# Performance work log

Hardware: AMD Instinct MI355X
Metric: run time of the kernel (lower is better)

The kernel has to match this reference:

```python
import jax, jax.numpy as jnp
import numpy as np

B, D_MODEL, N, H = 4, 256, 2048, 4
DIM = D_MODEL // H  # 64


def setup_inputs() -> dict:
    k = jax.random.key(0)
    ks = jax.random.split(k, 11)
    mk = lambda kk, shape, s=1.0: jax.random.normal(kk, shape, dtype=jnp.float32) * s
    return {
        'query': mk(ks[0], (B, D_MODEL, N)),
        'key': mk(ks[1], (B, D_MODEL, N)),
        'value': mk(ks[2], (B, D_MODEL, N)),
        # 1x1 Conv1d == per-position linear: weight [out, in], bias [out]
        'wq': mk(ks[3], (D_MODEL, D_MODEL), 0.05), 'bq': mk(ks[4], (D_MODEL,), 0.05),
        'wk': mk(ks[5], (D_MODEL, D_MODEL), 0.05), 'bk': mk(ks[6], (D_MODEL,), 0.05),
        'wv': mk(ks[7], (D_MODEL, D_MODEL), 0.05), 'bv': mk(ks[8], (D_MODEL,), 0.05),
        'wm': mk(ks[9], (D_MODEL, D_MODEL), 0.05), 'bm': mk(ks[10], (D_MODEL,), 0.05),
    }


def _proj(x, w, b):
    # Conv1d(kernel_size=1): [b, c_in, n] -> [b, c_out, n]
    return jnp.einsum('oc,bcn->bon', w, x) + b[None, :, None]


def reference(query, key, value, wq, bq, wk, bk, wv, bv, wm, bm):
    b = query.shape[0]
    # project and split channels d_model -> (dim, h); matches torch .view(b, dim, h, -1)
    q = _proj(query, wq, bq).reshape(b, DIM, H, -1)
    kk = _proj(key, wk, bk).reshape(b, DIM, H, -1)
    v = _proj(value, wv, bv).reshape(b, DIM, H, -1)
    scores = jnp.einsum('bdhn,bdhm->bhnm', q, kk) / jnp.sqrt(jnp.float32(DIM))
    prob = jax.nn.softmax(scores, axis=-1)  # [b, h, n, m]
    x = jnp.einsum('bhnm,bdhm->bdhn', prob, v)
    return _proj(x.reshape(b, DIM * H, -1), wm, bm)
```

## Files before the change

kernel.cpp:

```cpp
#include <hip/hip_runtime.h>
#include <hip/hip_bf16.h>

#define DMODEL 256
#define NSEQ   2048
#define NB     4
#define NH     4
#define DHEAD  64

typedef __attribute__((ext_vector_type(8))) short short8;
typedef __attribute__((ext_vector_type(4))) float float4v;
typedef __attribute__((ext_vector_type(2))) float float2v;
typedef __attribute__((ext_vector_type(2))) unsigned int uint2v;
typedef unsigned short u16;

#define AS1 __attribute__((address_space(1)))
#define AS3 __attribute__((address_space(3)))

static __device__ inline u16 f2bf(float f) {
    unsigned u = __builtin_bit_cast(unsigned, f);
    u += 0x7fffu + ((u >> 16) & 1u);
    return (u16)(u >> 16);
}
static __device__ inline unsigned pack2bf(float a, float b) {
    return (unsigned)f2bf(a) | ((unsigned)f2bf(b) << 16);
}
static __device__ inline float max3f(float a, float b, float c) {
    return fmaxf(fmaxf(a, b), c);
}
static __device__ inline float tmax16(const float4v* s) {
    float a = max3f(s[0][0], s[0][1], s[0][2]);
    float b = max3f(s[0][3], s[1][0], s[1][1]);
    float c = max3f(s[1][2], s[1][3], s[2][0]);
    float d = max3f(s[2][1], s[2][2], s[2][3]);
    float e = max3f(s[3][0], s[3][1], s[3][2]);
    float f = max3f(a, b, c);
    float g = max3f(d, e, s[3][3]);
    return fmaxf(f, g);
}

__global__ __launch_bounds__(256) void prep_kernel(
    const float* __restrict__ xq, const float* __restrict__ xk,
    const float* __restrict__ xv,
    const float* __restrict__ wq, const float* __restrict__ wk,
    const float* __restrict__ wv, const float* __restrict__ wm,
    u16* __restrict__ xt_ws, u16* __restrict__ wbf)
{
    const int bid = blockIdx.x;
    const int tid = threadIdx.x;

    if (bid >= 1536) {
        const int id = bid - 1536;
        const int sr = id & 255, m = id >> 8;
        const float* W = (m == 0) ? wq : (m == 1) ? wk : (m == 2) ? wv : wm;
        float v;
        if (m < 3) {
            int og = (sr & ~15) | ((sr & 3) << 2) | ((sr >> 2) & 3);
            v = W[(size_t)og * DMODEL + tid];
        } else {
            int c = ((tid & 63) << 2) | (tid >> 6);
            v = W[(size_t)sr * DMODEL + c];
        }
        wbf[(size_t)m * 65536 + (size_t)sr * DMODEL + tid] = f2bf(v);
        return;
    }

    const int nt = bid & 31;
    const int ct = (bid >> 5) & 3;
    const int z  = bid >> 7;
    const int b = z / 3, mode = z % 3;
    const float* X = ((mode == 0) ? xq : (mode == 1) ? xk : xv) + (size_t)b * DMODEL * NSEQ;
    u16* dst = xt_ws + (size_t)z * NSEQ * DMODEL;

    __shared__ u16 t[64][72];

    #pragma unroll
    for (int i = 0; i < 4; i++) {
        int e = tid + i * 256;
        int c = e >> 4;
        int n4 = (e & 15) * 4;
        float4v v = *(const float4v*)&X[(size_t)(ct * 64 + c) * NSEQ + nt * 64 + n4];
        #pragma unroll
        for (int j = 0; j < 4; j++) {
            int row = n4 + j;
            int fr = (row & 7) ^ ((row >> 3) & 7);
            t[row][(((c >> 3) ^ fr) << 3) + (c & 7)] = f2bf(v[j]);
        }
    }
    __syncthreads();
    #pragma unroll
    for (int i = 0; i < 4; i++) {
        int e = tid + i * 256;
        int n = e >> 4;
        int cb = (e & 15) * 4;
        int fr = (n & 7) ^ ((n >> 3) & 7);
        uint2v val = *(const uint2v*)&t[n][(((cb >> 3) ^ fr) << 3) + (cb & 7)];
        *(uint2v*)&dst[(size_t)(nt * 64 + n) * DMODEL + ct * 64 + cb] = val;
    }
}

__global__ __launch_bounds__(256) void proj_qkv_kernel(
    const u16* __restrict__ xt_ws, const u16* __restrict__ wbf,
    const float* __restrict__ bqp, const float* __restrict__ bkp, const float* __restrict__ bvp,
    u16* __restrict__ q_ws, u16* __restrict__ k_ws, u16* __restrict__ vt_ws)
{
    const int nt0 = blockIdx.x, ot = blockIdx.y, bz = blockIdx.z;
    const int b = bz / 3, mode = bz % 3;
    const float* BI = (mode == 0) ? bqp : (mode == 1) ? bkp : bvp;

    const int tid = threadIdx.x;
    const int wave = tid >> 6, lane = tid & 63;
    const int g = lane >> 4, ql = lane & 15;
    const int srow8 = lane >> 3, su = lane & 7;
    const int u_l = su ^ srow8;
    const int obase = ot * 64, nbase = nt0 * 64;

    const u16* Asrc = wbf + (size_t)mode * 65536;
    const u16* Bsrc = xt_ws + (size_t)bz * (NSEQ * DMODEL);

    __shared__ u16 at[2][64][64];
    __shared__ u16 bt[2][64][64];

    float4v acc[4];
    #pragma unroll
    for (int i = 0; i < 4; i++) acc[i] = (float4v){0.f, 0.f, 0.f, 0.f};

    #define PSTAGE(bufi_, c0_)                                                         \
        { _Pragma("unroll")                                                            \
          for (int p_ = 0; p_ < 2; p_++) {                                             \
            int rb_ = wave * 8 + p_ * 32;                                              \
            int row_ = rb_ + srow8;                                                    \
            __builtin_amdgcn_global_load_lds(                                          \
                (const AS1 unsigned int*)(Asrc + (size_t)(obase + row_) * DMODEL + (c0_) + u_l * 8), \
                (AS3 unsigned int*)&at[bufi_][rb_][0], 16, 0, 0);                      \
            __builtin_amdgcn_global_load_lds(                                          \
                (const AS1 unsigned int*)(Bsrc + (size_t)(nbase + row_) * DMODEL + (c0_) + u_l * 8), \
                (AS3 unsigned int*)&bt[bufi_][rb_][0], 16, 0, 0);                      \
          } }

    PSTAGE(0, 0)
    __syncthreads();
    int buf = 0;
    const int sw = ql & 7;
    #pragma unroll
    for (int t = 0; t < 4; t++) {
        if (t < 3) PSTAGE(buf ^ 1, (t + 1) * 64)
        #pragma unroll
        for (int kc = 0; kc < 2; kc++) {
            short8 afrag = *(const short8*)&at[buf][wave * 16 + ql][(((kc * 4 + g) ^ sw)) * 8];
            #pragma unroll
            for (int nt = 0; nt < 4; nt++) {
                short8 bfrag = *(const short8*)&bt[buf][nt * 16 + ql][(((kc * 4 + g) ^ sw)) * 8];
                acc[nt] = __builtin_amdgcn_mfma_f32_16x16x32_bf16(afrag, bfrag, acc[nt], 0, 0, 0);
            }
        }
        __syncthreads();
        buf ^= 1;
    }
    #undef PSTAGE

    const int h = g;
    const int d0 = (obase + wave * 16) >> 2;
    float bias[4];
    #pragma unroll
    for (int r = 0; r < 4; r++) bias[r] = BI[obase + wave * 16 + 4 * r + g];

    #pragma unroll
    for (int nt = 0; nt < 4; nt++) {
        int n = nbase + nt * 16 + ql;
        float v[4];
        #pragma unroll
        for (int r = 0; r < 4; r++) v[r] = acc[nt][r] + bias[r];
        if (mode == 0) {
            #pragma unroll
            for (int r = 0; r < 4; r++) v[r] *= 0.18033688011112042f;
            uint2v pk = {pack2bf(v[0], v[1]), pack2bf(v[2], v[3])};
            *(uint2v*)&q_ws[((size_t)(b * NH + h) * NSEQ + n) * DHEAD + d0] = pk;
        } else if (mode == 1) {
            uint2v pk = {pack2bf(v[0], v[1]), pack2bf(v[2], v[3])};
            *(uint2v*)&k_ws[((size_t)(b * NH + h) * NSEQ + n) * DHEAD + d0] = pk;
        } else {
            #pragma unroll
            for (int r = 0; r < 4; r++)
                vt_ws[((size_t)(b * NH + h) * DHEAD + d0 + r) * NSEQ + n] = f2bf(v[r]);
        }
    }
}

__global__ __launch_bounds__(512) void attn_kernel(
    const u16* __restrict__ q_ws, const u16* __restrict__ k_ws,
    const u16* __restrict__ vt_ws, float* __restrict__ part_ws,
    float* __restrict__ ml_ws)
{
    const int bid = blockIdx.x;
    const int orig = (bid & 7) * 64 + (bid >> 3);
    const int bh = orig >> 5;
    const int qt128 = (orig >> 1) & 15;
    const int half = orig & 1;
    const int tid = threadIdx.x;
    const int wave = tid >> 6, lane = tid & 63;
    const int g = lane >> 4, ql = lane & 15;
    const int qbase = qt128 * 128 + wave * 16;

    const u16* qp = q_ws + ((size_t)bh * NSEQ + qbase) * DHEAD;
    const u16* kp = k_ws + (size_t)bh * NSEQ * DHEAD + (size_t)half * 1024 * DHEAD;
    const u16* vp = vt_ws + (size_t)bh * DHEAD * NSEQ;
    const int voff = half * 1024;

    __shared__ u16 kt[2][64][64];
    __shared__ u16 vt[2][64][64];
    __shared__ u16 p_lds[8][16][72];

    const int srow = lane >> 3;
    const int su_l = lane & 7;
    const int u_l  = su_l ^ srow;
    const int swz  = ql & 7;

    short8 qf[2];
    #pragma unroll
    for (int kc = 0; kc < 2; kc++)
        qf[kc] = *(const short8*)(qp + (size_t)ql * DHEAD + kc * 32 + g * 8);

    float4v acc[4];
    #pragma unroll
    for (int t = 0; t < 4; t++) acc[t] = (float4v){0.f, 0.f, 0.f, 0.f};
    float mrun = -INFINITY, lrun = 0.f;

    #define STAGE(mb_, bufi_)                                                          \
        {                                                                              \
            int row_ = wave * 8 + srow;                                                \
            __builtin_amdgcn_global_load_lds(                                          \
                (const AS1 unsigned int*)(kp + (size_t)((mb_) + row_) * DHEAD + u_l * 8), \
                (AS3 unsigned int*)&kt[bufi_][wave * 8][0], 16, 0, 0);                 \
            __builtin_amdgcn_global_load_lds(                                          \
                (const AS1 unsigned int*)(vp + (size_t)row_ * NSEQ + voff + (mb_) + u_l * 8), \
                (AS3 unsigned int*)&vt[bufi_][wave * 8][0], 16, 0, 0);                 \
        }

    STAGE(0, 0);
    __syncthreads();

    int buf = 0;
    for (int t = 0; t < 16; t++) {
        const int mb = t * 64;
        if (t < 15) STAGE(mb + 64, buf ^ 1);

        float4v st[4];
        #pragma unroll
        for (int mt = 0; mt < 4; mt++) st[mt] = (float4v){0.f, 0.f, 0.f, 0.f};
        #pragma unroll
        for (int mt = 0; mt < 4; mt++) {
            #pragma unroll
            for (int kc = 0; kc < 2; kc++) {
                short8 kf = *(const short8*)&kt[buf][mt * 16 + ql][((kc * 4 + g) ^ swz) * 8];
                st[mt] = __builtin_amdgcn_mfma_f32_16x16x32_bf16(kf, qf[kc], st[mt], 0, 0, 0);
            }
        }

        float tmax = tmax16(&st[0]);
        tmax = fmaxf(tmax, __shfl_xor(tmax, 16, 64));
        tmax = fmaxf(tmax, __shfl_xor(tmax, 32, 64));

        if (__any(tmax > mrun + 8.f)) {
            float mnew = fmaxf(mrun, tmax);
            float a = __builtin_amdgcn_exp2f(mrun - mnew);
            #pragma unroll
            for (int tt = 0; tt < 4; tt++)
                #pragma unroll
                for (int r = 0; r < 4; r++) acc[tt][r] *= a;
            lrun *= a;
            mrun = mnew;
        }

        float psum = 0.f;
        #pragma unroll
        for (int mt = 0; mt < 4; mt++) {
            float p0 = __builtin_amdgcn_exp2f(st[mt][0] - mrun);
            float p1 = __builtin_amdgcn_exp2f(st[mt][1] - mrun);
            float p2 = __builtin_amdgcn_exp2f(st[mt][2] - mrun);
            float p3 = __builtin_amdgcn_exp2f(st[mt][3] - mrun);
            psum += (p0 + p1) + (p2 + p3);
            *(uint2v*)&p_lds[wave][ql][mt * 16 + g * 4] = (uint2v){pack2bf(p0, p1), pack2bf(p2, p3)};
        }
        psum += __shfl_xor(psum, 16, 64);
        psum += __shfl_xor(psum, 32, 64);
        lrun += psum;

        #pragma unroll
        for (int kc = 0; kc < 2; kc++) {
            short8 pf = *(const short8*)&p_lds[wave][ql][kc * 32 + g * 8];
            #pragma unroll
            for (int tt = 0; tt < 4; tt++) {
                short8 vf = *(const short8*)&vt[buf][tt * 16 + ql][((kc * 4 + g) ^ swz) * 8];
                acc[tt] = __builtin_amdgcn_mfma_f32_16x16x32_bf16(vf, pf, acc[tt], 0, 0, 0);
            }
        }
        __syncthreads();
        buf ^= 1;
    }
    #undef STAGE

    float* prow = part_ws + ((size_t)(half * 16 + bh) * NSEQ + qbase + ql) * 64;
    #pragma unroll
    for (int t = 0; t < 4; t++)
        *(float4v*)&prow[t * 16 + g * 4] = acc[t];
    if (g == 0) {
        *(float2v*)&ml_ws[((size_t)(half * 16 + bh) * NSEQ + qbase + ql) * 2] =
            (float2v){mrun, lrun};
    }
}

__global__ __launch_bounds__(256) void proj_out_kernel(
    const float* __restrict__ part_ws, const float* __restrict__ ml_ws,
    const u16* __restrict__ wbf, const float* __restrict__ bm,
    float* __restrict__ out)
{
    const int nt0 = blockIdx.x, ot = blockIdx.y, b = blockIdx.z;

    const int tid = threadIdx.x;
    const int wave = tid >> 6, lane = tid & 63;
    const int g = lane >> 4, ql = lane & 15;
    const int srow8 = lane >> 3, su = lane & 7;
    const int u_l = su ^ srow8;
    const int obase = ot * 64, nbase = nt0 * 64;

    const u16* Asrc = wbf + (size_t)3 * 65536;

    __shared__ u16 at[64][64];
    __shared__ u16 bt[64][64];

    float4v acc[4];
    #pragma unroll
    for (int i = 0; i < 4; i++) acc[i] = (float4v){0.f, 0.f, 0.f, 0.f};

    const int rrow = tid >> 2;
    const int qcol = tid & 3;
    const int sw = ql & 7;

    #pragma unroll
    for (int t = 0; t < 4; t++) {
        const int c0 = t * 64;
        __syncthreads();
        #pragma unroll
        for (int p_ = 0; p_ < 2; p_++) {
            int rb_ = wave * 8 + p_ * 32;
            int row_ = rb_ + srow8;
            __builtin_amdgcn_global_load_lds(
                (const AS1 unsigned int*)(Asrc + (size_t)(obase + row_) * DMODEL + c0 + u_l * 8),
                (AS3 unsigned int*)&at[rb_][0], 16, 0, 0);
        }
        {
            const int bh = b * NH + t;
            const int n = nbase + rrow;
            const float* p0 = part_ws + ((size_t)bh * NSEQ + n) * 64;
            const float* p1 = part_ws + ((size_t)(16 + bh) * NSEQ + n) * 64;
            float2v ml0 = *(const float2v*)&ml_ws[((size_t)bh * NSEQ + n) * 2];
            float2v ml1 = *(const float2v*)&ml_ws[((size_t)(16 + bh) * NSEQ + n) * 2];
            float mM = fmaxf(ml0[0], ml1[0]);
            float e0 = __builtin_amdgcn_exp2f(ml0[0] - mM);
            float e1 = __builtin_amdgcn_exp2f(ml1[0] - mM);
            float inv = 1.f / (ml0[1] * e0 + ml1[1] * e1);
            float s0 = e0 * inv, s1 = e1 * inv;
            #pragma unroll
            for (int j = 0; j < 4; j++) {
                int cb = qcol * 16 + j * 4;
                float4v f0 = *(const float4v*)&p0[cb];
                float4v f1 = *(const float4v*)&p1[cb];
                float x0 = f0[0] * s0 + f1[0] * s1;
                float x1 = f0[1] * s0 + f1[1] * s1;
                float x2 = f0[2] * s0 + f1[2] * s1;
                float x3 = f0[3] * s0 + f1[3] * s1;
                *(uint2v*)&bt[rrow][(((cb >> 3) ^ (rrow & 7)) << 3) + (cb & 7)] =
                    (uint2v){pack2bf(x0, x1), pack2bf(x2, x3)};
            }
        }
        __syncthreads();
        #pragma unroll
        for (int kc = 0; kc < 2; kc++) {
            short8 afrag = *(const short8*)&at[wave * 16 + ql][(((kc * 4 + g) ^ sw)) * 8];
            #pragma unroll
            for (int nt = 0; nt < 4; nt++) {
                short8 bfrag = *(const short8*)&bt[nt * 16 + ql][(((kc * 4 + g) ^ sw)) * 8];
                acc[nt] = __builtin_amdgcn_mfma_f32_16x16x32_bf16(afrag, bfrag, acc[nt], 0, 0, 0);
            }
        }
    }

    const int o0 = obase + wave * 16 + g * 4;
    #pragma unroll
    for (int nt = 0; nt < 4; nt++) {
        int n = nbase + nt * 16 + ql;
        #pragma unroll
        for (int r = 0; r < 4; r++) {
            int o = o0 + r;
            out[((size_t)b * DMODEL + o) * NSEQ + n] = acc[nt][r] + bm[o];
        }
    }
}

extern "C" void kernel_launch(void* const* d_in, const int* in_sizes, int n_in,
                              void* d_out, int out_size, void* d_ws, size_t ws_size,
                              hipStream_t stream)
{
    const float* query = (const float*)d_in[0];
    const float* key   = (const float*)d_in[1];
    const float* value = (const float*)d_in[2];
    const float* wq = (const float*)d_in[3];
    const float* bq = (const float*)d_in[4];
    const float* wk = (const float*)d_in[5];
    const float* bk = (const float*)d_in[6];
    const float* wv = (const float*)d_in[7];
    const float* bv = (const float*)d_in[8];
    const float* wm = (const float*)d_in[9];
    const float* bm = (const float*)d_in[10];
    float* out = (float*)d_out;

    char* ws = (char*)d_ws;
    const size_t SEG = (size_t)NB * NH * NSEQ * DHEAD * sizeof(u16);
    u16*   q_ws    = (u16*)(ws);
    u16*   k_ws    = (u16*)(ws + SEG);
    u16*   vt_ws   = (u16*)(ws + 2 * SEG);
    float* part_ws = (float*)(ws + 3 * SEG);
    float* ml_ws   = (float*)(ws + 3 * SEG + (size_t)2 * 16 * NSEQ * 64 * sizeof(float));
    char*  after_ml = ws + 3 * SEG + (size_t)2 * 16 * NSEQ * 64 * sizeof(float)
                         + (size_t)2 * 16 * NSEQ * 2 * sizeof(float);
    u16*   xt_ws   = (u16*)(after_ml);
    u16*   wbf     = (u16*)(after_ml + (size_t)12 * NSEQ * DMODEL * sizeof(u16));

    prep_kernel<<<dim3(2560), 256, 0, stream>>>(
        query, key, value, wq, wk, wv, wm, xt_ws, wbf);
    proj_qkv_kernel<<<dim3(32, 4, 12), 256, 0, stream>>>(
        xt_ws, wbf, bq, bk, bv, q_ws, k_ws, vt_ws);
    attn_kernel<<<dim3(512), 512, 0, stream>>>(q_ws, k_ws, vt_ws, part_ws, ml_ws);
    proj_out_kernel<<<dim3(32, 4, NB), 256, 0, stream>>>(part_ws, ml_ws, wbf, bm, out);
}
```

Before: 146.4 us.

## Split KV into quarters and give each wave two query tiles

The attention kernel now splits the key sequence four ways instead of two and launches 1024 blocks of 4 waves instead of 512 blocks of 8 waves. Each wave handles 32 query rows as two 16-row tiles, so every K/V fragment read from LDS feeds two MFMAs. The output projection merges four partial softmax results instead of two. The aim is better LDS reuse and more parallelism, at the cost of twice the partial-result traffic, a larger workspace and more registers per wave.

Measured after the change: 160.4 us. 9.5% more time.

```diff
diff --git a/kernel.cpp b/kernel.cpp
--- a/kernel.cpp
+++ b/kernel.cpp
@@ -186,112 +186,140 @@
     }
 }
 
-__global__ __launch_bounds__(512) void attn_kernel(
+__global__ __launch_bounds__(256) void attn_kernel(
     const u16* __restrict__ q_ws, const u16* __restrict__ k_ws,
     const u16* __restrict__ vt_ws, float* __restrict__ part_ws,
     float* __restrict__ ml_ws)
 {
     const int bid = blockIdx.x;
-    const int orig = (bid & 7) * 64 + (bid >> 3);
-    const int bh = orig >> 5;
-    const int qt128 = (orig >> 1) & 15;
-    const int half = orig & 1;
+    const int orig = (bid & 7) * 128 + (bid >> 3);
+    const int bh = orig >> 6;
+    const int qt128 = (orig >> 2) & 15;
+    const int quarter = orig & 3;
     const int tid = threadIdx.x;
     const int wave = tid >> 6, lane = tid & 63;
     const int g = lane >> 4, ql = lane & 15;
-    const int qbase = qt128 * 128 + wave * 16;
+    const int qbase = qt128 * 128 + wave * 32;
 
     const u16* qp = q_ws + ((size_t)bh * NSEQ + qbase) * DHEAD;
-    const u16* kp = k_ws + (size_t)bh * NSEQ * DHEAD + (size_t)half * 1024 * DHEAD;
+    const u16* kp = k_ws + (size_t)bh * NSEQ * DHEAD + (size_t)quarter * 512 * DHEAD;
     const u16* vp = vt_ws + (size_t)bh * DHEAD * NSEQ;
-    const int voff = half * 1024;
+    const int voff = quarter * 512;
 
     __shared__ u16 kt[2][64][64];
     __shared__ u16 vt[2][64][64];
-    __shared__ u16 p_lds[8][16][72];
+    __shared__ u16 p_lds[4][2][16][72];
 
     const int srow = lane >> 3;
     const int su_l = lane & 7;
     const int u_l  = su_l ^ srow;
     const int swz  = ql & 7;
 
-    short8 qf[2];
-    #pragma unroll
-    for (int kc = 0; kc < 2; kc++)
-        qf[kc] = *(const short8*)(qp + (size_t)ql * DHEAD + kc * 32 + g * 8);
-
-    float4v acc[4];
-    #pragma unroll
-    for (int t = 0; t < 4; t++) acc[t] = (float4v){0.f, 0.f, 0.f, 0.f};
-    float mrun = -INFINITY, lrun = 0.f;
+    short8 qf[2][2];
+    #pragma unroll
+    for (int qt = 0; qt < 2; qt++)
+        #pragma unroll
+        for (int kc = 0; kc < 2; kc++)
+            qf[qt][kc] = *(const short8*)(qp + (size_t)(qt * 16 + ql) * DHEAD + kc * 32 + g * 8);
+
+    float4v acc[2][4];
+    #pragma unroll
+    for (int qt = 0; qt < 2; qt++)
+        #pragma unroll
+        for (int t = 0; t < 4; t++) acc[qt][t] = (float4v){0.f, 0.f, 0.f, 0.f};
+    float m0 = -INFINITY, m1 = -INFINITY, l0 = 0.f, l1 = 0.f;
 
     #define STAGE(mb_, bufi_)                                                          \
         {                                                                              \
-            int row_ = wave * 8 + srow;                                                \
-            __builtin_amdgcn_global_load_lds(                                          \
-                (const AS1 unsigned int*)(kp + (size_t)((mb_) + row_) * DHEAD + u_l * 8), \
-                (AS3 unsigned int*)&kt[bufi_][wave * 8][0], 16, 0, 0);                 \
-            __builtin_amdgcn_global_load_lds(                                          \
-                (const AS1 unsigned int*)(vp + (size_t)row_ * NSEQ + voff + (mb_) + u_l * 8), \
-                (AS3 unsigned int*)&vt[bufi_][wave * 8][0], 16, 0, 0);                 \
+            _Pragma("unroll")                                                          \
+            for (int i_ = 0; i_ < 2; i_++) {                                           \
+                int row_ = wave * 16 + i_ * 8 + srow;                                  \
+                __builtin_amdgcn_global_load_lds(                                      \
+                    (const AS1 unsigned int*)(kp + (size_t)((mb_) + row_) * DHEAD + u_l * 8), \
+                    (AS3 unsigned int*)&kt[bufi_][wave * 16 + i_ * 8][0], 16, 0, 0);   \
+                __builtin_amdgcn_global_load_lds(                                      \
+                    (const AS1 unsigned int*)(vp + (size_t)row_ * NSEQ + voff + (mb_) + u_l * 8), \
+                    (AS3 unsigned int*)&vt[bufi_][wave * 16 + i_ * 8][0], 16, 0, 0);   \
+            }                                                                          \
         }
 
     STAGE(0, 0);
     __syncthreads();
 
     int buf = 0;
-    for (int t = 0; t < 16; t++) {
+    for (int t = 0; t < 8; t++) {
         const int mb = t * 64;
-        if (t < 15) STAGE(mb + 64, buf ^ 1);
-
-        float4v st[4];
-        #pragma unroll
-        for (int mt = 0; mt < 4; mt++) st[mt] = (float4v){0.f, 0.f, 0.f, 0.f};
+        if (t < 7) STAGE(mb + 64, buf ^ 1);
+
+        float4v st[2][4];
+        #pragma unroll
+        for (int qt = 0; qt < 2; qt++)
+            #pragma unroll
+            for (int mt = 0; mt < 4; mt++) st[qt][mt] = (float4v){0.f, 0.f, 0.f, 0.f};
         #pragma unroll
         for (int mt = 0; mt < 4; mt++) {
             #pragma unroll
             for (int kc = 0; kc < 2; kc++) {
                 short8 kf = *(const short8*)&kt[buf][mt * 16 + ql][((kc * 4 + g) ^ swz) * 8];
-                st[mt] = __builtin_amdgcn_mfma_f32_16x16x32_bf16(kf, qf[kc], st[mt], 0, 0, 0);
-            }
-        }
-
-        float tmax = tmax16(&st[0]);
-        tmax = fmaxf(tmax, __shfl_xor(tmax, 16, 64));
-        tmax = fmaxf(tmax, __shfl_xor(tmax, 32, 64));
-
-        if (__any(tmax > mrun + 8.f)) {
-            float mnew = fmaxf(mrun, tmax);
-            float a = __builtin_amdgcn_exp2f(mrun - mnew);
+                st[0][mt] = __builtin_amdgcn_mfma_f32_16x16x32_bf16(kf, qf[0][kc], st[0][mt], 0, 0, 0);
+                st[1][mt] = __builtin_amdgcn_mfma_f32_16x16x32_bf16(kf, qf[1][kc], st[1][mt], 0, 0, 0);
+            }
+        }
+
+        float tmax0 = tmax16(&st[0][0]);
+        float tmax1 = tmax16(&st[1][0]);
+        tmax0 = fmaxf(tmax0, __shfl_xor(tmax0, 16, 64));
+        tmax0 = fmaxf(tmax0, __shfl_xor(tmax0, 32, 64));
+        tmax1 = fmaxf(tmax1, __shfl_xor(tmax1, 16, 64));
+        tmax1 = fmaxf(tmax1, __shfl_xor(tmax1, 32, 64));
+
+        bool need = (tmax0 > m0 + 8.f) || (tmax1 > m1 + 8.f);
+        if (__any(need)) {
+            float mn0 = fmaxf(m0, tmax0), mn1 = fmaxf(m1, tmax1);
+            float a0 = __builtin_amdgcn_exp2f(m0 - mn0);
+            float a1 = __builtin_amdgcn_exp2f(m1 - mn1);
             #pragma unroll
             for (int tt = 0; tt < 4; tt++)
                 #pragma unroll
-                for (int r = 0; r < 4; r++) acc[tt][r] *= a;
-            lrun *= a;
-            mrun = mnew;
-        }
-
-        float psum = 0.f;
+                for (int r = 0; r < 4; r++) {
+                    acc[0][tt][r] *= a0;
+                    acc[1][tt][r] *= a1;
+                }
+            l0 *= a0; l1 *= a1;
+            m0 = mn0; m1 = mn1;
+        }
+
+        float ps0 = 0.f, ps1 = 0.f;
         #pragma unroll
         for (int mt = 0; mt < 4; mt++) {
-            float p0 = __builtin_amdgcn_exp2f(st[mt][0] - mrun);
-            float p1 = __builtin_amdgcn_exp2f(st[mt][1] - mrun);
-            float p2 = __builtin_amdgcn_exp2f(st[mt][2] - mrun);
-            float p3 = __builtin_amdgcn_exp2f(st[mt][3] - mrun);
-            psum += (p0 + p1) + (p2 + p3);
-            *(uint2v*)&p_lds[wave][ql][mt * 16 + g * 4] = (uint2v){pack2bf(p0, p1), pack2bf(p2, p3)};
-        }
-        psum += __shfl_xor(psum, 16, 64);
-        psum += __shfl_xor(psum, 32, 64);
-        lrun += psum;
+            float p00 = __builtin_amdgcn_exp2f(st[0][mt][0] - m0);
+            float p01 = __builtin_amdgcn_exp2f(st[0][mt][1] - m0);
+            float p02 = __builtin_amdgcn_exp2f(st[0][mt][2] - m0);
+            float p03 = __builtin_amdgcn_exp2f(st[0][mt][3] - m0);
+            ps0 += (p00 + p01) + (p02 + p03);
+            *(uint2v*)&p_lds[wave][0][ql][mt * 16 + g * 4] = (uint2v){pack2bf(p00, p01), pack2bf(p02, p03)};
+            float p10 = __builtin_amdgcn_exp2f(st[1][mt][0] - m1);
+            float p11 = __builtin_amdgcn_exp2f(st[1][mt][1] - m1);
+            float p12 = __builtin_amdgcn_exp2f(st[1][mt][2] - m1);
+            float p13 = __builtin_amdgcn_exp2f(st[1][mt][3] - m1);
+            ps1 += (p10 + p11) + (p12 + p13);
+            *(uint2v*)&p_lds[wave][1][ql][mt * 16 + g * 4] = (uint2v){pack2bf(p10, p11), pack2bf(p12, p13)};
+        }
+        ps0 += __shfl_xor(ps0, 16, 64);
+        ps0 += __shfl_xor(ps0, 32, 64);
+        ps1 += __shfl_xor(ps1, 16, 64);
+        ps1 += __shfl_xor(ps1, 32, 64);
+        l0 += ps0; l1 += ps1;
 
         #pragma unroll
         for (int kc = 0; kc < 2; kc++) {
-            short8 pf = *(const short8*)&p_lds[wave][ql][kc * 32 + g * 8];
+            short8 pf0 = *(const short8*)&p_lds[wave][0][ql][kc * 32 + g * 8];
+            short8 pf1 = *(const short8*)&p_lds[wave][1][ql][kc * 32 + g * 8];
             #pragma unroll
             for (int tt = 0; tt < 4; tt++) {
                 short8 vf = *(const short8*)&vt[buf][tt * 16 + ql][((kc * 4 + g) ^ swz) * 8];
-                acc[tt] = __builtin_amdgcn_mfma_f32_16x16x32_bf16(vf, pf, acc[tt], 0, 0, 0);
+                acc[0][tt] = __builtin_amdgcn_mfma_f32_16x16x32_bf16(vf, pf0, acc[0][tt], 0, 0, 0);
+                acc[1][tt] = __builtin_amdgcn_mfma_f32_16x16x32_bf16(vf, pf1, acc[1][tt], 0, 0, 0);
             }
         }
         __syncthreads();
@@ -299,13 +327,16 @@
     }
     #undef STAGE
 
-    float* prow = part_ws + ((size_t)(half * 16 + bh) * NSEQ + qbase + ql) * 64;
-    #pragma unroll
-    for (int t = 0; t < 4; t++)
-        *(float4v*)&prow[t * 16 + g * 4] = acc[t];
-    if (g == 0) {
-        *(float2v*)&ml_ws[((size_t)(half * 16 + bh) * NSEQ + qbase + ql) * 2] =
-            (float2v){mrun, lrun};
+    #pragma unroll
+    for (int qt = 0; qt < 2; qt++) {
+        float* prow = part_ws + ((size_t)(quarter * 16 + bh) * NSEQ + qbase + qt * 16 + ql) * 64;
+        #pragma unroll
+        for (int t = 0; t < 4; t++)
+            *(float4v*)&prow[t * 16 + g * 4] = acc[qt][t];
+        if (g == 0) {
+            *(float2v*)&ml_ws[((size_t)(quarter * 16 + bh) * NSEQ + qbase + qt * 16 + ql) * 2] =
+                (float2v){qt ? m1 : m0, qt ? l1 : l0};
+        }
     }
 }
 
@@ -351,24 +382,34 @@
         {
             const int bh = b * NH + t;
             const int n = nbase + rrow;
-            const float* p0 = part_ws + ((size_t)bh * NSEQ + n) * 64;
-            const float* p1 = part_ws + ((size_t)(16 + bh) * NSEQ + n) * 64;
-            float2v ml0 = *(const float2v*)&ml_ws[((size_t)bh * NSEQ + n) * 2];
-            float2v ml1 = *(const float2v*)&ml_ws[((size_t)(16 + bh) * NSEQ + n) * 2];
-            float mM = fmaxf(ml0[0], ml1[0]);
-            float e0 = __builtin_amdgcn_exp2f(ml0[0] - mM);
-            float e1 = __builtin_amdgcn_exp2f(ml1[0] - mM);
-            float inv = 1.f / (ml0[1] * e0 + ml1[1] * e1);
-            float s0 = e0 * inv, s1 = e1 * inv;
+            float ms[4], ls[4];
+            #pragma unroll
+            for (int s = 0; s < 4; s++) {
+                float2v ml = *(const float2v*)&ml_ws[((size_t)(s * 16 + bh) * NSEQ + n) * 2];
+                ms[s] = ml[0]; ls[s] = ml[1];
+            }
+            float mM = fmaxf(fmaxf(ms[0], ms[1]), fmaxf(ms[2], ms[3]));
+            float e0 = __builtin_amdgcn_exp2f(ms[0] - mM);
+            float e1 = __builtin_amdgcn_exp2f(ms[1] - mM);
+            float e2 = __builtin_amdgcn_exp2f(ms[2] - mM);
+            float e3 = __builtin_amdgcn_exp2f(ms[3] - mM);
+            float inv = 1.f / (ls[0] * e0 + ls[1] * e1 + ls[2] * e2 + ls[3] * e3);
+            float s0 = e0 * inv, s1 = e1 * inv, s2 = e2 * inv, s3 = e3 * inv;
+            const float* p0 = part_ws + ((size_t)(0 * 16 + bh) * NSEQ + n) * 64;
+            const float* p1 = part_ws + ((size_t)(1 * 16 + bh) * NSEQ + n) * 64;
+            const float* p2 = part_ws + ((size_t)(2 * 16 + bh) * NSEQ + n) * 64;
+            const float* p3 = part_ws + ((size_t)(3 * 16 + bh) * NSEQ + n) * 64;
             #pragma unroll
             for (int j = 0; j < 4; j++) {
                 int cb = qcol * 16 + j * 4;
                 float4v f0 = *(const float4v*)&p0[cb];
                 float4v f1 = *(const float4v*)&p1[cb];
-                float x0 = f0[0] * s0 + f1[0] * s1;
-                float x1 = f0[1] * s0 + f1[1] * s1;
-                float x2 = f0[2] * s0 + f1[2] * s1;
-                float x3 = f0[3] * s0 + f1[3] * s1;
+                float4v f2 = *(const float4v*)&p2[cb];
+                float4v f3 = *(const float4v*)&p3[cb];
+                float x0 = f0[0] * s0 + f1[0] * s1 + f2[0] * s2 + f3[0] * s3;
+                float x1 = f0[1] * s0 + f1[1] * s1 + f2[1] * s2 + f3[1] * s3;
+                float x2 = f0[2] * s0 + f1[2] * s1 + f2[2] * s2 + f3[2] * s3;
+                float x3 = f0[3] * s0 + f1[3] * s1 + f2[3] * s2 + f3[3] * s3;
                 *(uint2v*)&bt[rrow][(((cb >> 3) ^ (rrow & 7)) << 3) + (cb & 7)] =
                     (uint2v){pack2bf(x0, x1), pack2bf(x2, x3)};
             }
@@ -420,9 +461,9 @@
     u16*   k_ws    = (u16*)(ws + SEG);
     u16*   vt_ws   = (u16*)(ws + 2 * SEG);
     float* part_ws = (float*)(ws + 3 * SEG);
-    float* ml_ws   = (float*)(ws + 3 * SEG + (size_t)2 * 16 * NSEQ * 64 * sizeof(float));
-    char*  after_ml = ws + 3 * SEG + (size_t)2 * 16 * NSEQ * 64 * sizeof(float)
-                         + (size_t)2 * 16 * NSEQ * 2 * sizeof(float);
+    float* ml_ws   = (float*)(ws + 3 * SEG + (size_t)4 * 16 * NSEQ * 64 * sizeof(float));
+    char*  after_ml = ws + 3 * SEG + (size_t)4 * 16 * NSEQ * 64 * sizeof(float)
+                         + (size_t)4 * 16 * NSEQ * 2 * sizeof(float);
     u16*   xt_ws   = (u16*)(after_ml);
     u16*   wbf     = (u16*)(after_ml + (size_t)12 * NSEQ * DMODEL * sizeof(u16));
 
@@ -430,6 +471,6 @@
         query, key, value, wq, wk, wv, wm, xt_ws, wbf);
     proj_qkv_kernel<<<dim3(32, 4, 12), 256, 0, stream>>>(
         xt_ws, wbf, bq, bk, bv, q_ws, k_ws, vt_ws);
-    attn_kernel<<<dim3(512), 512, 0, stream>>>(q_ws, k_ws, vt_ws, part_ws, ml_ws);
+    attn_kernel<<<dim3(1024), 256, 0, stream>>>(q_ws, k_ws, vt_ws, part_ws, ml_ws);
     proj_out_kernel<<<dim3(32, 4, NB), 256, 0, stream>>>(part_ws, ml_ws, wbf, bm, out);
 }
```
